# Kernel tuning notes

Hardware: AMD Instinct MI355X
Metric: run time of the kernel (lower is better)

The kernel has to match this reference:

```python
import jax, jax.numpy as jnp
import numpy as np

B, N, D, K, H, HID, ITERS = 16, 4096, 64, 8, 4, 256, 3
DH = D // H
EPS = 1e-5


def _ln(x, g, b):
    m = x.mean(-1, keepdims=True)
    v = x.var(-1, keepdims=True)
    return (x - m) / jnp.sqrt(v + EPS) * g + b


def setup_inputs() -> dict:
    ks = jax.random.split(jax.random.key(0), 16)
    s = 1.0 / np.sqrt(D)
    return {
        "embeddings": jax.random.normal(ks[0], (B, N, D), dtype=jnp.float32),
        "slots_mu": jax.random.normal(ks[1], (1, K, D), dtype=jnp.float32) * 0.1,
        "slots_logsigma": jax.random.normal(ks[2], (1, K, D), dtype=jnp.float32) * 0.1,
        "mixing_init": jnp.full((1, K), 1.0 / K, dtype=jnp.float32),
        "to_keys": jax.random.uniform(ks[3], (K, D, D), dtype=jnp.float32),
        "to_queries": jax.random.uniform(ks[4], (K, D, D), dtype=jnp.float32),
        "to_values": jax.random.uniform(ks[5], (K, D, D), dtype=jnp.float32),
        "w_ih": jax.random.uniform(ks[6], (3 * D, D), minval=-s, maxval=s),
        "w_hh": jax.random.uniform(ks[7], (3 * D, D), minval=-s, maxval=s),
        "b_ih": jax.random.uniform(ks[8], (3 * D,), minval=-s, maxval=s),
        "b_hh": jax.random.uniform(ks[9], (3 * D,), minval=-s, maxval=s),
        "w1": jax.random.uniform(ks[10], (HID, D), minval=-s, maxval=s),
        "b1": jnp.zeros((HID,), jnp.float32),
        "w2": jax.random.uniform(ks[11], (D, HID), minval=-1.0 / np.sqrt(HID), maxval=1.0 / np.sqrt(HID)),
        "b2": jnp.zeros((D,), jnp.float32),
        "ln_in_g": jnp.ones((D,), jnp.float32), "ln_in_b": jnp.zeros((D,), jnp.float32),
        "ln_sl_g": jnp.ones((D,), jnp.float32), "ln_sl_b": jnp.zeros((D,), jnp.float32),
        "ln_ff_g": jnp.ones((D,), jnp.float32), "ln_ff_b": jnp.zeros((D,), jnp.float32),
        "noise_init": jax.random.normal(ks[12], (B, K, D), dtype=jnp.float32),
        "noise_final": jax.random.normal(ks[13], (B, K, D), dtype=jnp.float32),
    }


def reference(embeddings, slots_mu, slots_logsigma, mixing_init, to_keys, to_queries,
              to_values, w_ih, w_hh, b_ih, b_hh, w1, b1, w2, b2,
              ln_in_g, ln_in_b, ln_sl_g, ln_sl_b, ln_ff_g, ln_ff_b,
              noise_init, noise_final):
    mu = jnp.broadcast_to(slots_mu, (B, K, D))
    sigma = jnp.broadcast_to(jnp.exp(slots_logsigma), (B, K, D))
    slots = mu + sigma * noise_init                              # [B,K,D]
    mixing = jnp.broadcast_to(mixing_init, (B, K))[:, :, None]   # [B,K,1]

    x = _ln(embeddings, ln_in_g, ln_in_b)                        # [B,N,D]
    keys = jnp.einsum('bne,ked->bknd', x, to_keys).reshape(B, K, N, H, DH)
    values = jnp.einsum('bne,ked->bknd', x, to_values).reshape(B, K, N, H, DH)
    sigma = sigma.reshape(B, K, H, DH)
    # torch.einsum('bkd,kdd->bkd') uses the DIAGONAL of to_queries
    qdiag = jnp.einsum('kdd->kd', to_queries)                    # [K,D]
    log_pi = -0.5 * D * np.log(2.0 * np.pi)

    attn_vis = None
    for _ in range(ITERS):
        slots_prev = slots
        s_ln = _ln(slots, ln_sl_g, ln_sl_b)
        queries = (s_ln * qdiag[None]).reshape(B, K, H, DH)      # [B,K,H,Dh]
        exponent = -0.5 * (keys - queries[:, :, None]) ** 2 / (sigma[:, :, None] ** 2 + EPS)
        log_scale = -jnp.log(jnp.clip(sigma, EPS, None))[:, :, None]  # [B,K,1,H,Dh]
        gll = jnp.log(mixing + EPS)[..., None] + (log_pi + log_scale + exponent).sum(-1)  # [B,K,N,H]
        attn = jax.nn.softmax(gll, axis=1) + EPS
        attn_vis = attn
        Nk = attn.sum(axis=(2, 3))[:, :, None]                   # [B,K,1]
        upd = jnp.einsum('bknh,bknhd->bkhd', attn, values).reshape(B, K, D)
        upd = (1.0 / Nk + EPS) * upd
        nq = upd.reshape(B, K, H, DH)                            # source overwrites new_queries with slot_updates
        sig2 = jnp.einsum('bknh,bknhd->bkhd', attn, (keys - nq[:, :, None]) ** 2).reshape(B, K, D)
        sigma = (jnp.sqrt(sig2 / Nk) + EPS).reshape(B, K, H, DH)
        mixing = Nk / N
        # GRUCell (torch gate order: reset, update, new)
        xg = upd.reshape(-1, D) @ w_ih.T + b_ih
        hg = slots_prev.reshape(-1, D) @ w_hh.T + b_hh
        xr, xz, xn = jnp.split(xg, 3, axis=-1)
        hr, hz, hn = jnp.split(hg, 3, axis=-1)
        r = jax.nn.sigmoid(xr + hr)
        z = jax.nn.sigmoid(xz + hz)
        n = jnp.tanh(xn + r * hn)
        slots = ((1.0 - z) * n + z * slots_prev.reshape(-1, D)).reshape(B, K, D)
        pre = _ln(slots, ln_ff_g, ln_ff_b)
        slots = slots + jax.nn.relu(pre @ w1.T + b1) @ w2.T + b2

    sigma = sigma.reshape(B, K, D)
    slots = slots + sigma * noise_final
    return slots, attn_vis
```

## Files before the change

kernel.cpp:

```cpp
#include <hip/hip_runtime.h>
#include <math.h>

#define B_ 16
#define N_ 4096
#define D_ 64
#define K_ 8
#define H_ 4
#define HID_ 256
#define ITERS_ 3
#define EPS_ 1e-5f

#define PREC_ 3104
#define NBLK_ 64

#define HTERM_ (-940.9930580015849f)

__device__ __forceinline__ float waveReduceSum64(float v) {
  v += __shfl_xor(v, 1);  v += __shfl_xor(v, 2);  v += __shfl_xor(v, 4);
  v += __shfl_xor(v, 8);  v += __shfl_xor(v, 16); v += __shfl_xor(v, 32);
  return v;
}
__device__ __forceinline__ float groupReduceSum16(float v) {
  v += __shfl_xor(v, 1); v += __shfl_xor(v, 2); v += __shfl_xor(v, 4);
  v += __shfl_xor(v, 8);
  return v;
}

template <int CTRL>
__device__ __forceinline__ float dpp_mov(float v) {
  return __int_as_float(__builtin_amdgcn_update_dpp(
      0, __float_as_int(v), CTRL, 0xF, 0xF, true));
}
__device__ __forceinline__ float row16Sum(float v) {
  v += dpp_mov<0xB1>(v);
  v += dpp_mov<0x4E>(v);
  v += dpp_mov<0x124>(v);
  v += dpp_mov<0x128>(v);
  return v;
}

__global__ void ln_emb_kernel(const float* __restrict__ emb,
                              const float* __restrict__ g, const float* __restrict__ b,
                              float* __restrict__ x, int b0) {
  int wave = threadIdx.x >> 6, lane = threadIdx.x & 63;
  int row = blockIdx.x * 4 + wave;
  float e = emb[((size_t)b0 * N_ + row) * 64 + lane];
  float s  = waveReduceSum64(e);
  float sq = waveReduceSum64(e * e);
  float mean = s * (1.0f / 64.0f);
  float var  = sq * (1.0f / 64.0f) - mean * mean;
  float inv  = rsqrtf(var + EPS_);
  x[(size_t)row * 64 + lane] = (e - mean) * inv * g[lane] + b[lane];
}

__global__ __launch_bounds__(256) void key_kernel(const float* __restrict__ x,
    const float* __restrict__ Wk, float* __restrict__ keys) {
  __shared__ float xst[64 * 68];
  __shared__ float wks[64 * 64];
  int n0 = blockIdx.x * 64;
  int bl = blockIdx.y;
  int tid = threadIdx.x;

  const float* xb = x + ((size_t)bl * N_ + n0) * 64;
  for (int i = tid; i < 4096; i += 256) {
    int n = i >> 6, e = i & 63;
    xst[e * 68 + n] = xb[i];
  }

  int tr = tid >> 4, tc = tid & 15;
  int r0 = tr * 4, c0 = tc * 4;
  size_t outb = ((size_t)bl * N_ + n0) * 512;

  for (int k = 0; k < K_; ++k) {
    __syncthreads();
    const float4* wk4 = (const float4*)(Wk + (size_t)k * 4096);
    float4* wks4 = (float4*)wks;
    for (int i = tid; i < 1024; i += 256) wks4[i] = wk4[i];
    __syncthreads();

    float ak[4][4] = {{0.f}};
    #pragma unroll 8
    for (int kk = 0; kk < 64; ++kk) {
      float4 xq = *(const float4*)&xst[kk * 68 + r0];
      float4 wq = *(const float4*)&wks[kk * 64 + c0];
      float xv[4] = {xq.x, xq.y, xq.z, xq.w};
      float wc[4] = {wq.x, wq.y, wq.z, wq.w};
      #pragma unroll
      for (int i = 0; i < 4; ++i)
        #pragma unroll
        for (int j = 0; j < 4; ++j)
          ak[i][j] = fmaf(xv[i], wc[j], ak[i][j]);
    }
    size_t ob = outb + (size_t)k * 64;
    #pragma unroll
    for (int i = 0; i < 4; ++i) {
      float4 kq = make_float4(ak[i][0], ak[i][1], ak[i][2], ak[i][3]);
      *(float4*)&keys[ob + (size_t)(r0 + i) * 512 + c0] = kq;
    }
  }
}

__global__ void init_kernel(const float* __restrict__ mu, const float* __restrict__ lsig,
                            const float* __restrict__ mix0, const float* __restrict__ noise,
                            const float* __restrict__ tq,
                            const float* __restrict__ g_sl, const float* __restrict__ b_sl,
                            float* __restrict__ slots, float* __restrict__ q,
                            float* __restrict__ i2s, float* __restrict__ base, int b0) {
  int bk = b0 * K_ + blockIdx.x;
  int lane = threadIdx.x;
  int k = bk & (K_ - 1);
  int kd = k * 64 + lane;
  float sg = expf(lsig[kd]);
  float s = mu[kd] + sg * noise[bk * 64 + lane];
  slots[bk * 64 + lane] = s;
  float su = waveReduceSum64(s);
  float sq = waveReduceSum64(s * s);
  float mean = su * (1.0f / 64.0f);
  float var  = sq * (1.0f / 64.0f) - mean * mean;
  float sl = (s - mean) * rsqrtf(var + EPS_) * g_sl[lane] + b_sl[lane];
  q[bk * 64 + lane] = sl * tq[k * 4096 + lane * 65];
  i2s[bk * 64 + lane] = 0.5f / (sg * sg + EPS_);
  float ls = -logf(fmaxf(sg, EPS_));
  float lss = groupReduceSum16(ls);
  if ((lane & 15) == 0)
    base[bk * 4 + (lane >> 4)] = logf(mix0[k] + EPS_) + HTERM_ + lss;
}

template <bool WRITE_ATTN>
__global__ __launch_bounds__(256, 4) void attn_kernel(
    const float* __restrict__ keys, const float* __restrict__ x,
    const float* __restrict__ q, const float* __restrict__ i2s, const float* __restrict__ base,
    float* __restrict__ P, float* __restrict__ attn_out, int b0) {
  int bl = blockIdx.y;
  int bg = b0 + bl;
  int wave = threadIdx.x >> 6, lane = threadIdx.x & 63;
  int h = lane >> 4;
  int n0 = (blockIdx.x * 4 + wave) * 16;

  __shared__ float att_lds[4][K_][64];
  __shared__ float blk[PREC_];
  __shared__ float bv_lds[32];
  for (int i = threadIdx.x; i < PREC_; i += 256) blk[i] = 0.0f;
  if (threadIdx.x < 32) bv_lds[threadIdx.x] = base[bg * 32 + threadIdx.x];

  float qv[K_], iv[K_];
  {
    const float* qp = q + bg * 512 + lane;
    const float* ip = i2s + bg * 512 + lane;
    #pragma unroll
    for (int k = 0; k < K_; ++k) { qv[k] = qp[k * 64]; iv[k] = ip[k * 64]; }
  }
  float s1a[K_] = {0.f}, s2a[K_] = {0.f};
  __syncthreads();

  const float* kptr = keys + ((size_t)bl * N_ + n0) * 512 + lane;
  #pragma unroll 2
  for (int ni = 0; ni < 16; ++ni) {
    float key[K_], gl[K_];
    #pragma unroll
    for (int k = 0; k < K_; ++k) key[k] = kptr[k * 64];
    #pragma unroll
    for (int k = 0; k < K_; ++k) {
      float df = key[k] - qv[k];
      float t = row16Sum(df * df * iv[k]);
      gl[k] = bv_lds[k * 4 + h] - t;
    }
    float m = gl[0];
    #pragma unroll
    for (int k = 1; k < K_; ++k) m = fmaxf(m, gl[k]);
    float ssum = 0.f;
    #pragma unroll
    for (int k = 0; k < K_; ++k) { gl[k] = __expf(gl[k] - m); ssum += gl[k]; }
    float inv = __builtin_amdgcn_rcpf(ssum);
    #pragma unroll
    for (int k = 0; k < K_; ++k) {
      float a = gl[k] * inv + EPS_;
      s1a[k] = fmaf(a, key[k], s1a[k]);
      s2a[k] = fmaf(a * key[k], key[k], s2a[k]);
      if ((lane & 15) == 0) att_lds[wave][k][ni * 4 + h] = a;
    }
    kptr += 512;
  }
  #pragma unroll
  for (int k = 0; k < K_; ++k) {
    atomicAdd(&blk[k * 64 + lane],       s1a[k]);
    atomicAdd(&blk[512 + k * 64 + lane], s2a[k]);
  }

  float xr[16];
  {
    const float* xptr = x + ((size_t)bl * N_ + n0) * 64 + lane;
    #pragma unroll
    for (int ni = 0; ni < 16; ++ni) xr[ni] = xptr[ni * 64];
  }
  #pragma unroll
  for (int k = 0; k < K_; ++k) {
    float t0 = 0.f, t1 = 0.f, t2 = 0.f, t3 = 0.f;
    float c0 = 0.f, c1 = 0.f, c2 = 0.f, c3 = 0.f;
    #pragma unroll
    for (int ni = 0; ni < 16; ++ni) {
      float4 a4 = *(const float4*)&att_lds[wave][k][ni * 4];
      float xv = xr[ni];
      t0 = fmaf(a4.x, xv, t0); t1 = fmaf(a4.y, xv, t1);
      t2 = fmaf(a4.z, xv, t2); t3 = fmaf(a4.w, xv, t3);
      c0 += a4.x; c1 += a4.y; c2 += a4.z; c3 += a4.w;
    }
    atomicAdd(&blk[1024 + k * 256 + lane],       t0);
    atomicAdd(&blk[1024 + k * 256 + 64 + lane],  t1);
    atomicAdd(&blk[1024 + k * 256 + 128 + lane], t2);
    atomicAdd(&blk[1024 + k * 256 + 192 + lane], t3);
    if (lane == 0) {
      atomicAdd(&blk[3072 + k * 4 + 0], c0);
      atomicAdd(&blk[3072 + k * 4 + 1], c1);
      atomicAdd(&blk[3072 + k * 4 + 2], c2);
      atomicAdd(&blk[3072 + k * 4 + 3], c3);
    }
  }
  __syncthreads();
  {
    float4* p4 = (float4*)(P + ((size_t)bl * NBLK_ + blockIdx.x) * PREC_);
    const float4* b4 = (const float4*)blk;
    for (int i = threadIdx.x; i < PREC_ / 4; i += 256) p4[i] = b4[i];
  }
  if (WRITE_ATTN) {
    #pragma unroll
    for (int k = 0; k < K_; ++k)
      attn_out[((size_t)(bg * K_ + k) * N_ + n0) * 4 + lane] = att_lds[wave][k][lane];
  }
}

__global__ __launch_bounds__(256) void update_kernel(
    const float* __restrict__ P, const float* __restrict__ Wv,
    float* __restrict__ slots,
    const float* __restrict__ w_ih, const float* __restrict__ w_hh,
    const float* __restrict__ b_ih, const float* __restrict__ b_hh,
    const float* __restrict__ w1, const float* __restrict__ b1,
    const float* __restrict__ w2, const float* __restrict__ b2,
    const float* __restrict__ g_ff, const float* __restrict__ b_ff,
    const float* __restrict__ tq,
    const float* __restrict__ g_sl, const float* __restrict__ b_sl,
    float* __restrict__ q, float* __restrict__ i2s, float* __restrict__ base,
    const float* __restrict__ noise_final, float* __restrict__ out_slots,
    int last, int b0) {
  int bx = blockIdx.x;
  int bl = bx >> 3;
  int bk = b0 * K_ + bx;
  int k = bx & (K_ - 1);
  int t = threadIdx.x;
  __shared__ float S1_s[64], S2_s[64], T_s[256], S0_s[4];
  __shared__ float upd_s[64], sp_s[64], sig_s[64], xg_s[192], hg_s[192],
                   snew_s[64], pre_s[64], hid_s[256];

  {
    int off0;
    if (t < 64)        off0 = k * 64 + t;
    else if (t < 128)  off0 = 512 + k * 64 + (t - 64);
    else               off0 = 1024 + k * 256 + (t - 128);
    int j1 = t + 256;
    int off1 = -1;
    if (j1 < 384)      off1 = 1024 + k * 256 + (j1 - 128);
    else if (j1 < 388) off1 = 3072 + k * 4 + (j1 - 384);
    float acc0 = 0.f, acc1 = 0.f;
    const float* Pb = P + (size_t)bl * NBLK_ * PREC_;
    #pragma unroll 4
    for (int a = 0; a < NBLK_; ++a) {
      const float* pa = Pb + (size_t)a * PREC_;
      acc0 += pa[off0];
      if (off1 >= 0) acc1 += pa[off1];
    }
    if (t < 64)       S1_s[t] = acc0;
    else if (t < 128) S2_s[t - 64] = acc0;
    else              T_s[t - 128] = acc0;
    if (t < 128)      T_s[t + 128] = acc1;
    else if (t < 132) S0_s[t - 128] = acc1;
  }
  __syncthreads();

  if (t < 64) {
    float nk = S0_s[0] + S0_s[1] + S0_s[2] + S0_s[3];
    float sv = 0.f;
    const float* Trow = &T_s[(t >> 4) * 64];
    const float* wv = Wv + (size_t)k * 4096 + t;
    #pragma unroll 8
    for (int e = 0; e < 64; ++e) sv = fmaf(Trow[e], wv[(size_t)e * 64], sv);
    float upd = (1.0f / nk + EPS_) * sv;
    upd_s[t] = upd;
    float s1 = S1_s[t], s2 = S2_s[t], s0 = S0_s[t >> 4];
    float sig2 = fmaxf(s2 - 2.0f * upd * s1 + upd * upd * s0, 0.0f);
    sig_s[t] = sqrtf(sig2 / nk) + EPS_;
    sp_s[t] = slots[bk * 64 + t];
  }
  __syncthreads();
  if (t < 192) {
    const float4* wr = (const float4*)(w_ih + t * 64);
    const float4* wh = (const float4*)(w_hh + t * 64);
    float a1 = b_ih[t], a2 = b_hh[t];
    #pragma unroll
    for (int d4 = 0; d4 < 16; ++d4) {
      float4 wa = wr[d4], wb = wh[d4];
      const float* u  = &upd_s[d4 * 4];
      const float* sp = &sp_s[d4 * 4];
      a1 += u[0] * wa.x + u[1] * wa.y + u[2] * wa.z + u[3] * wa.w;
      a2 += sp[0] * wb.x + sp[1] * wb.y + sp[2] * wb.z + sp[3] * wb.w;
    }
    xg_s[t] = a1;
    hg_s[t] = a2;
  }
  __syncthreads();
  if (t < 64) {
    float r = 1.0f / (1.0f + expf(-(xg_s[t] + hg_s[t])));
    float z = 1.0f / (1.0f + expf(-(xg_s[64 + t] + hg_s[64 + t])));
    float nn = tanhf(xg_s[128 + t] + r * hg_s[128 + t]);
    float sn = (1.0f - z) * nn + z * sp_s[t];
    snew_s[t] = sn;
    float su = waveReduceSum64(sn);
    float sq = waveReduceSum64(sn * sn);
    float mean = su * (1.0f / 64.0f);
    float var  = sq * (1.0f / 64.0f) - mean * mean;
    pre_s[t] = (sn - mean) * rsqrtf(var + EPS_) * g_ff[t] + b_ff[t];
  }
  __syncthreads();
  {
    const float4* w1r = (const float4*)(w1 + t * 64);
    float a = b1[t];
    #pragma unroll
    for (int d4 = 0; d4 < 16; ++d4) {
      float4 w = w1r[d4];
      const float* p = &pre_s[d4 * 4];
      a += p[0] * w.x + p[1] * w.y + p[2] * w.z + p[3] * w.w;
    }
    hid_s[t] = fmaxf(a, 0.0f);
  }
  __syncthreads();
  if (t < 64) {
    const float4* w2r = (const float4*)(w2 + t * 256);
    float a = b2[t];
    #pragma unroll
    for (int j4 = 0; j4 < 64; ++j4) {
      float4 w = w2r[j4];
      const float* p = &hid_s[j4 * 4];
      a += p[0] * w.x + p[1] * w.y + p[2] * w.z + p[3] * w.w;
    }
    float outv = snew_s[t] + a;
    slots[bk * 64 + t] = outv;
    if (last) {
      out_slots[bk * 64 + t] = outv + sig_s[t] * noise_final[bk * 64 + t];
    } else {
      float su = waveReduceSum64(outv);
      float sq = waveReduceSum64(outv * outv);
      float mean = su * (1.0f / 64.0f);
      float var  = sq * (1.0f / 64.0f) - mean * mean;
      float sl = (outv - mean) * rsqrtf(var + EPS_) * g_sl[t] + b_sl[t];
      q[bk * 64 + t] = sl * tq[k * 4096 + t * 65];
      float sg = sig_s[t];
      i2s[bk * 64 + t] = 0.5f / (sg * sg + EPS_);
      float ls = -logf(fmaxf(sg, EPS_));
      float lss = groupReduceSum16(ls);
      float nk = S0_s[0] + S0_s[1] + S0_s[2] + S0_s[3];
      if ((t & 15) == 0)
        base[bk * 4 + (t >> 4)] = logf(nk * (1.0f / (float)N_) + EPS_) + HTERM_ + lss;
    }
  }
}

extern "C" void kernel_launch(void* const* d_in, const int* in_sizes, int n_in,
                              void* d_out, int out_size, void* d_ws, size_t ws_size,
                              hipStream_t stream) {
  const float* emb  = (const float*)d_in[0];
  const float* mu   = (const float*)d_in[1];
  const float* lsig = (const float*)d_in[2];
  const float* mix0 = (const float*)d_in[3];
  const float* Wk   = (const float*)d_in[4];
  const float* Wq   = (const float*)d_in[5];
  const float* Wv   = (const float*)d_in[6];
  const float* w_ih = (const float*)d_in[7];
  const float* w_hh = (const float*)d_in[8];
  const float* b_ih = (const float*)d_in[9];
  const float* b_hh = (const float*)d_in[10];
  const float* w1   = (const float*)d_in[11];
  const float* b1   = (const float*)d_in[12];
  const float* w2   = (const float*)d_in[13];
  const float* b2   = (const float*)d_in[14];
  const float* g_in = (const float*)d_in[15];
  const float* b_in = (const float*)d_in[16];
  const float* g_sl = (const float*)d_in[17];
  const float* b_sl = (const float*)d_in[18];
  const float* g_ff = (const float*)d_in[19];
  const float* b_ff = (const float*)d_in[20];
  const float* nz0  = (const float*)d_in[21];
  const float* nzf  = (const float*)d_in[22];

  float* ws = (float*)d_ws;
  float* slots = ws;
  float* q     = slots + 8192;
  float* i2s   = q + 8192;
  float* base  = i2s + 8192;
  float* x     = base + 512;
  const size_t small_bytes = (size_t)(3 * 8192 + 512) * 4;
  const size_t per_batch = (size_t)(N_ * 64 + N_ * 512 + NBLK_ * PREC_) * 4;

  int C = 16;
  while (C > 1 && small_bytes + (size_t)C * per_batch > ws_size) C >>= 1;
  float* keys = x + (size_t)C * N_ * 64;
  float* P    = keys + (size_t)C * N_ * 512;

  float* out_slots = (float*)d_out;
  float* out_attn  = out_slots + B_ * K_ * 64;

  for (int b0 = 0; b0 < B_; b0 += C) {
    ln_emb_kernel<<<dim3(C * N_ / 4), 256, 0, stream>>>(emb, g_in, b_in, x, b0);
    key_kernel<<<dim3(N_ / 64, C), 256, 0, stream>>>(x, Wk, keys);
    init_kernel<<<dim3(C * K_), 64, 0, stream>>>(mu, lsig, mix0, nz0, Wq, g_sl, b_sl,
                                                 slots, q, i2s, base, b0);
    for (int it = 0; it < ITERS_; ++it) {
      int last = (it == ITERS_ - 1) ? 1 : 0;
      if (last)
        attn_kernel<true><<<dim3(NBLK_, C), 256, 0, stream>>>(keys, x, q, i2s, base,
                                                              P, out_attn, b0);
      else
        attn_kernel<false><<<dim3(NBLK_, C), 256, 0, stream>>>(keys, x, q, i2s, base,
                                                               P, nullptr, b0);
      update_kernel<<<dim3(C * K_), 256, 0, stream>>>(P, Wv, slots,
          w_ih, w_hh, b_ih, b_hh, w1, b1, w2, b2, g_ff, b_ff,
          Wq, g_sl, b_sl, q, i2s, base, nzf, out_slots, last, b0);
    }
  }
}
```

Before: 537.0 us.

## Fuse input layernorm into key kernel and reduce attention partials with global atomics

The embedding layernorm moves into the key projection kernel, so normalized rows go straight into shared memory and the separate launch and global re-read are gone. The attention kernel now accumulates its per-block partial sums (S1, S2, T, S0) into per-slot global accumulators with atomicAdd, replacing the per-block partial buffer that the update kernel had to reduce over 64 blocks. The update kernel reads the final sums directly and zeroes them for the next iteration, and init zeroes them first. In exchange there is atomic contention from 64 blocks per batch on the same addresses, and float-atomic ordering makes results nondeterministic.

```diff
diff --git a/kernel.cpp b/kernel.cpp
--- a/kernel.cpp
+++ b/kernel.cpp
@@ -10,9 +10,6 @@
 #define ITERS_ 3
 #define EPS_ 1e-5f
 
-#define PREC_ 3104
-#define NBLK_ 64
-
 #define HTERM_ (-940.9930580015849f)
 
 __device__ __forceinline__ float waveReduceSum64(float v) {
@@ -39,32 +36,32 @@
   return v;
 }
 
-__global__ void ln_emb_kernel(const float* __restrict__ emb,
-                              const float* __restrict__ g, const float* __restrict__ b,
-                              float* __restrict__ x, int b0) {
-  int wave = threadIdx.x >> 6, lane = threadIdx.x & 63;
-  int row = blockIdx.x * 4 + wave;
-  float e = emb[((size_t)b0 * N_ + row) * 64 + lane];
-  float s  = waveReduceSum64(e);
-  float sq = waveReduceSum64(e * e);
-  float mean = s * (1.0f / 64.0f);
-  float var  = sq * (1.0f / 64.0f) - mean * mean;
-  float inv  = rsqrtf(var + EPS_);
-  x[(size_t)row * 64 + lane] = (e - mean) * inv * g[lane] + b[lane];
-}
-
-__global__ __launch_bounds__(256) void key_kernel(const float* __restrict__ x,
-    const float* __restrict__ Wk, float* __restrict__ keys) {
+__global__ __launch_bounds__(256) void key_kernel(const float* __restrict__ emb,
+    const float* __restrict__ g_in, const float* __restrict__ b_in,
+    const float* __restrict__ Wk, float* __restrict__ x,
+    float* __restrict__ keys, int b0) {
   __shared__ float xst[64 * 68];
   __shared__ float wks[64 * 64];
   int n0 = blockIdx.x * 64;
   int bl = blockIdx.y;
   int tid = threadIdx.x;
-
-  const float* xb = x + ((size_t)bl * N_ + n0) * 64;
-  for (int i = tid; i < 4096; i += 256) {
-    int n = i >> 6, e = i & 63;
-    xst[e * 68 + n] = xb[i];
+  int wave = tid >> 6, lane = tid & 63;
+
+  {
+    const float* eb = emb + ((size_t)(b0 + bl) * N_ + n0 + wave * 16) * 64 + lane;
+    float* xrow = x + ((size_t)bl * N_ + n0 + wave * 16) * 64 + lane;
+    float gl = g_in[lane], bb = b_in[lane];
+    #pragma unroll 4
+    for (int r = 0; r < 16; ++r) {
+      float e = eb[(size_t)r * 64];
+      float s  = waveReduceSum64(e);
+      float sq = waveReduceSum64(e * e);
+      float mean = s * (1.0f / 64.0f);
+      float var  = sq * (1.0f / 64.0f) - mean * mean;
+      float xv = (e - mean) * rsqrtf(var + EPS_) * gl + bb;
+      xst[lane * 68 + wave * 16 + r] = xv;
+      xrow[(size_t)r * 64] = xv;
+    }
   }
 
   int tr = tid >> 4, tc = tid & 15;
@@ -105,7 +102,9 @@
                             const float* __restrict__ tq,
                             const float* __restrict__ g_sl, const float* __restrict__ b_sl,
                             float* __restrict__ slots, float* __restrict__ q,
-                            float* __restrict__ i2s, float* __restrict__ base, int b0) {
+                            float* __restrict__ i2s, float* __restrict__ base,
+                            float* __restrict__ S1, float* __restrict__ S2,
+                            float* __restrict__ S0, float* __restrict__ T, int b0) {
   int bk = b0 * K_ + blockIdx.x;
   int lane = threadIdx.x;
   int k = bk & (K_ - 1);
@@ -124,13 +123,21 @@
   float lss = groupReduceSum16(ls);
   if ((lane & 15) == 0)
     base[bk * 4 + (lane >> 4)] = logf(mix0[k] + EPS_) + HTERM_ + lss;
+  S1[bk * 64 + lane] = 0.0f;
+  S2[bk * 64 + lane] = 0.0f;
+  T[bk * 256 + lane]       = 0.0f;
+  T[bk * 256 + 64 + lane]  = 0.0f;
+  T[bk * 256 + 128 + lane] = 0.0f;
+  T[bk * 256 + 192 + lane] = 0.0f;
+  if (lane < 4) S0[bk * 4 + lane] = 0.0f;
 }
 
 template <bool WRITE_ATTN>
 __global__ __launch_bounds__(256, 4) void attn_kernel(
     const float* __restrict__ keys, const float* __restrict__ x,
     const float* __restrict__ q, const float* __restrict__ i2s, const float* __restrict__ base,
-    float* __restrict__ P, float* __restrict__ attn_out, int b0) {
+    float* __restrict__ S1, float* __restrict__ S2, float* __restrict__ S0,
+    float* __restrict__ T, float* __restrict__ attn_out, int b0) {
   int bl = blockIdx.y;
   int bg = b0 + bl;
   int wave = threadIdx.x >> 6, lane = threadIdx.x & 63;
@@ -138,9 +145,9 @@
   int n0 = (blockIdx.x * 4 + wave) * 16;
 
   __shared__ float att_lds[4][K_][64];
-  __shared__ float blk[PREC_];
+  __shared__ float blk[3104];
   __shared__ float bv_lds[32];
-  for (int i = threadIdx.x; i < PREC_; i += 256) blk[i] = 0.0f;
+  for (int i = threadIdx.x; i < 3104; i += 256) blk[i] = 0.0f;
   if (threadIdx.x < 32) bv_lds[threadIdx.x] = base[bg * 32 + threadIdx.x];
 
   float qv[K_], iv[K_];
@@ -217,11 +224,13 @@
     }
   }
   __syncthreads();
-  {
-    float4* p4 = (float4*)(P + ((size_t)bl * NBLK_ + blockIdx.x) * PREC_);
-    const float4* b4 = (const float4*)blk;
-    for (int i = threadIdx.x; i < PREC_ / 4; i += 256) p4[i] = b4[i];
-  }
+  for (int i = threadIdx.x; i < 512; i += 256) {
+    atomicAdd(&S1[bg * 512 + i], blk[i]);
+    atomicAdd(&S2[bg * 512 + i], blk[512 + i]);
+  }
+  for (int i = threadIdx.x; i < 2048; i += 256)
+    atomicAdd(&T[bg * 2048 + i], blk[1024 + i]);
+  if (threadIdx.x < 32) atomicAdd(&S0[bg * 32 + threadIdx.x], blk[3072 + threadIdx.x]);
   if (WRITE_ATTN) {
     #pragma unroll
     for (int k = 0; k < K_; ++k)
@@ -230,7 +239,9 @@
 }
 
 __global__ __launch_bounds__(256) void update_kernel(
-    const float* __restrict__ P, const float* __restrict__ Wv,
+    float* __restrict__ S1, float* __restrict__ S2,
+    float* __restrict__ S0, float* __restrict__ T,
+    const float* __restrict__ Wv,
     float* __restrict__ slots,
     const float* __restrict__ w_ih, const float* __restrict__ w_hh,
     const float* __restrict__ b_ih, const float* __restrict__ b_hh,
@@ -242,53 +253,32 @@
     float* __restrict__ q, float* __restrict__ i2s, float* __restrict__ base,
     const float* __restrict__ noise_final, float* __restrict__ out_slots,
     int last, int b0) {
-  int bx = blockIdx.x;
-  int bl = bx >> 3;
-  int bk = b0 * K_ + bx;
-  int k = bx & (K_ - 1);
+  int bk = b0 * K_ + blockIdx.x;
+  int k = bk & (K_ - 1);
   int t = threadIdx.x;
-  __shared__ float S1_s[64], S2_s[64], T_s[256], S0_s[4];
   __shared__ float upd_s[64], sp_s[64], sig_s[64], xg_s[192], hg_s[192],
                    snew_s[64], pre_s[64], hid_s[256];
-
-  {
-    int off0;
-    if (t < 64)        off0 = k * 64 + t;
-    else if (t < 128)  off0 = 512 + k * 64 + (t - 64);
-    else               off0 = 1024 + k * 256 + (t - 128);
-    int j1 = t + 256;
-    int off1 = -1;
-    if (j1 < 384)      off1 = 1024 + k * 256 + (j1 - 128);
-    else if (j1 < 388) off1 = 3072 + k * 4 + (j1 - 384);
-    float acc0 = 0.f, acc1 = 0.f;
-    const float* Pb = P + (size_t)bl * NBLK_ * PREC_;
-    #pragma unroll 4
-    for (int a = 0; a < NBLK_; ++a) {
-      const float* pa = Pb + (size_t)a * PREC_;
-      acc0 += pa[off0];
-      if (off1 >= 0) acc1 += pa[off1];
-    }
-    if (t < 64)       S1_s[t] = acc0;
-    else if (t < 128) S2_s[t - 64] = acc0;
-    else              T_s[t - 128] = acc0;
-    if (t < 128)      T_s[t + 128] = acc1;
-    else if (t < 132) S0_s[t - 128] = acc1;
-  }
-  __syncthreads();
-
+  float nk = 0.f;
   if (t < 64) {
-    float nk = S0_s[0] + S0_s[1] + S0_s[2] + S0_s[3];
+    nk = S0[bk * 4 + 0] + S0[bk * 4 + 1] + S0[bk * 4 + 2] + S0[bk * 4 + 3];
     float sv = 0.f;
-    const float* Trow = &T_s[(t >> 4) * 64];
+    const float* Trow = T + bk * 256 + (t >> 4) * 64;
     const float* wv = Wv + (size_t)k * 4096 + t;
     #pragma unroll 8
     for (int e = 0; e < 64; ++e) sv = fmaf(Trow[e], wv[(size_t)e * 64], sv);
     float upd = (1.0f / nk + EPS_) * sv;
     upd_s[t] = upd;
-    float s1 = S1_s[t], s2 = S2_s[t], s0 = S0_s[t >> 4];
+    float s1 = S1[bk * 64 + t], s2 = S2[bk * 64 + t], s0 = S0[bk * 4 + (t >> 4)];
     float sig2 = fmaxf(s2 - 2.0f * upd * s1 + upd * upd * s0, 0.0f);
     sig_s[t] = sqrtf(sig2 / nk) + EPS_;
     sp_s[t] = slots[bk * 64 + t];
+    S1[bk * 64 + t] = 0.0f;
+    S2[bk * 64 + t] = 0.0f;
+    T[bk * 256 + t]       = 0.0f;
+    T[bk * 256 + 64 + t]  = 0.0f;
+    T[bk * 256 + 128 + t] = 0.0f;
+    T[bk * 256 + 192 + t] = 0.0f;
+    if (t < 4) S0[bk * 4 + t] = 0.0f;
   }
   __syncthreads();
   if (t < 192) {
@@ -356,7 +346,6 @@
       i2s[bk * 64 + t] = 0.5f / (sg * sg + EPS_);
       float ls = -logf(fmaxf(sg, EPS_));
       float lss = groupReduceSum16(ls);
-      float nk = S0_s[0] + S0_s[1] + S0_s[2] + S0_s[3];
       if ((t & 15) == 0)
         base[bk * 4 + (t >> 4)] = logf(nk * (1.0f / (float)N_) + EPS_) + HTERM_ + lss;
     }
@@ -395,32 +384,34 @@
   float* q     = slots + 8192;
   float* i2s   = q + 8192;
   float* base  = i2s + 8192;
-  float* x     = base + 512;
-  const size_t small_bytes = (size_t)(3 * 8192 + 512) * 4;
-  const size_t per_batch = (size_t)(N_ * 64 + N_ * 512 + NBLK_ * PREC_) * 4;
+  float* S1    = base + 512;
+  float* S2    = S1 + 8192;
+  float* S0    = S2 + 8192;
+  float* T     = S0 + 512;
+  float* x     = T + 32768;
+  const size_t small_bytes = (size_t)(5 * 8192 + 2 * 512 + 32768) * 4;
+  const size_t per_batch = (size_t)(N_ * 64 + N_ * 512) * 4;
 
   int C = 16;
   while (C > 1 && small_bytes + (size_t)C * per_batch > ws_size) C >>= 1;
   float* keys = x + (size_t)C * N_ * 64;
-  float* P    = keys + (size_t)C * N_ * 512;
 
   float* out_slots = (float*)d_out;
   float* out_attn  = out_slots + B_ * K_ * 64;
 
   for (int b0 = 0; b0 < B_; b0 += C) {
-    ln_emb_kernel<<<dim3(C * N_ / 4), 256, 0, stream>>>(emb, g_in, b_in, x, b0);
-    key_kernel<<<dim3(N_ / 64, C), 256, 0, stream>>>(x, Wk, keys);
+    key_kernel<<<dim3(N_ / 64, C), 256, 0, stream>>>(emb, g_in, b_in, Wk, x, keys, b0);
     init_kernel<<<dim3(C * K_), 64, 0, stream>>>(mu, lsig, mix0, nz0, Wq, g_sl, b_sl,
-                                                 slots, q, i2s, base, b0);
+                                                 slots, q, i2s, base, S1, S2, S0, T, b0);
     for (int it = 0; it < ITERS_; ++it) {
       int last = (it == ITERS_ - 1) ? 1 : 0;
       if (last)
-        attn_kernel<true><<<dim3(NBLK_, C), 256, 0, stream>>>(keys, x, q, i2s, base,
-                                                              P, out_attn, b0);
+        attn_kernel<true><<<dim3(N_ / 64, C), 256, 0, stream>>>(keys, x, q, i2s, base,
+                                                                S1, S2, S0, T, out_attn, b0);
       else
-        attn_kernel<false><<<dim3(NBLK_, C), 256, 0, stream>>>(keys, x, q, i2s, base,
-                                                               P, nullptr, b0);
-      update_kernel<<<dim3(C * K_), 256, 0, stream>>>(P, Wv, slots,
+        attn_kernel<false><<<dim3(N_ / 64, C), 256, 0, stream>>>(keys, x, q, i2s, base,
+                                                                 S1, S2, S0, T, nullptr, b0);
+      update_kernel<<<dim3(C * K_), 256, 0, stream>>>(S1, S2, S0, T, Wv, slots,
           w_ih, w_hh, b_ih, b_hh, w1, b1, w2, b2, g_ff, b_ff,
           Wq, g_sl, b_sl, q, i2s, base, nzf, out_slots, last, b0);
     }
```

Result: faster. 473.8 us (-11.8%).
